# Kernel tuning notes

Hardware: AMD Instinct MI355X
Metric: run time of the kernel (lower is better)

Reference implementation:

```python
import jax, jax.numpy as jnp
import numpy as np

N_NODES = 10000
N_EDGES = 160000
N_FEAT = 512
HEADS = 8
HID = 128
OUT = 16


def setup_inputs() -> dict:
    key = jax.random.key(0)
    ks = jax.random.split(key, 16)
    inp = {
        'node_features': jax.random.normal(ks[0], (N_NODES, N_FEAT), jnp.float32),
        'edge_src': jax.random.randint(ks[1], (N_EDGES,), 0, N_NODES, jnp.int32),
        'edge_dst': jax.random.randint(ks[2], (N_EDGES,), 0, N_NODES, jnp.int32),
        # GAT layer params (scaled randn for numerical sanity)
        'W1': jax.random.normal(ks[3], (HEADS, HID, N_FEAT), jnp.float32) * 0.05,
        'a1': jax.random.normal(ks[4], (HEADS, 2 * HID), jnp.float32) * 0.05,
        'W2': jax.random.normal(ks[5], (HEADS, HID, HID), jnp.float32) * 0.05,
        'a2': jax.random.normal(ks[6], (HEADS, 2 * HID), jnp.float32) * 0.05,
        # MLP: LayerNorm(128) -> Linear(128,64) -> LeakyReLU -> Linear(64,16) -> LeakyReLU -> Linear(16,OUT) -> ReLU
        'ln_g': jnp.ones((HID,), jnp.float32),
        'ln_b': jnp.zeros((HID,), jnp.float32),
        'Wl1': jax.random.normal(ks[7], (64, HID), jnp.float32) * 0.05,
        'bl1': jnp.zeros((64,), jnp.float32),
        'Wl2': jax.random.normal(ks[8], (16, 64), jnp.float32) * 0.05,
        'bl2': jnp.zeros((16,), jnp.float32),
        'Wl3': jax.random.normal(ks[9], (OUT, 16), jnp.float32) * 0.05,
        'bl3': jnp.zeros((OUT,), jnp.float32),
    }
    return inp


def gat_layer(x, src, dst, W, a, n_nodes):
    # per-node, per-head projection: h[n,h,d]
    h = jnp.einsum('hdf,nf->nhd', W, x)
    # split attention vector: e_ij = a[:HID].h_i + a[HID:].h_j
    s_i = jnp.einsum('nhd,hd->nh', h, a[:, :HID])  # score contribution of target i
    s_j = jnp.einsum('nhd,hd->nh', h, a[:, HID:])  # score contribution of neighbor j
    e = jax.nn.leaky_relu(s_i[dst] + s_j[src])     # [E,H], negative_slope=0.01 (torch default)
    # segment softmax over edges grouped by dst
    m = jax.ops.segment_max(e, dst, num_segments=n_nodes)           # [N,H]
    m = jnp.where(jnp.isfinite(m), m, 0.0)
    ex = jnp.exp(e - m[dst])                                        # [E,H]
    denom = jax.ops.segment_sum(ex, dst, num_segments=n_nodes)      # [N,H]
    alpha = ex / jnp.where(denom > 0, denom, 1.0)[dst]              # [E,H]
    # scatter-accumulate weighted neighbor embeddings
    agg = jax.ops.segment_sum(alpha[:, :, None] * h[src], dst, num_segments=n_nodes)  # [N,H,HID]
    # average over heads, ELU (matches 1/attn_heads * attn_sum -> ELU)
    return jax.nn.elu(agg.mean(axis=1))  # [N,HID]


def reference(node_features, edge_src, edge_dst, W1, a1, W2, a2,
              ln_g, ln_b, Wl1, bl1, Wl2, bl2, Wl3, bl3):
    n = node_features.shape[0]
    emb1 = gat_layer(node_features, edge_src, edge_dst, W1, a1, n)
    emb2 = gat_layer(emb1, edge_src, edge_dst, W2, a2, n)
    g = emb2.mean(axis=0)  # [HID] graph embedding
    # MLP head (dropout = identity at inference)
    mu = g.mean()
    var = ((g - mu) ** 2).mean()
    gn = (g - mu) / jnp.sqrt(var + 1e-5) * ln_g + ln_b
    x = jax.nn.leaky_relu(Wl1 @ gn + bl1)
    x = jax.nn.leaky_relu(Wl2 @ x + bl2)
    return jax.nn.relu(Wl3 @ x + bl3)
```

## Files before the change

kernel.cpp:

```cpp
#include <hip/hip_runtime.h>
#include <math.h>

#define N_NODES 10000
#define N_EDGES 160000
#define N_FEAT  512
#define HEADS   8
#define HID     128

typedef __attribute__((ext_vector_type(8))) short bf16x8;
typedef __attribute__((ext_vector_type(4))) float f32x4;
typedef __attribute__((ext_vector_type(2))) float v2f;

__device__ inline unsigned short f2bf_rne(float f) {
  unsigned int u = __float_as_uint(f);
  unsigned int r = u + 0x7fffu + ((u >> 16) & 1u);
  return (unsigned short)(r >> 16);
}
__device__ inline float bf2f(unsigned int b) {
  return __uint_as_float(b << 16);
}

__device__ inline void split_body(const float* __restrict__ in,
                                  unsigned short* __restrict__ hi,
                                  int R, int K8, int idx) {
  int r = idx & 15;
  int t = idx >> 4;
  int kq = t % K8;
  int rb = t / K8;
  int row = rb * 16 + r;
  float v[8] = {0.f, 0.f, 0.f, 0.f, 0.f, 0.f, 0.f, 0.f};
  if (row < R) {
    const float* p = in + (size_t)row * (K8 * 8) + kq * 8;
    float4 a = *(const float4*)p;
    float4 b = *(const float4*)(p + 4);
    v[0] = a.x; v[1] = a.y; v[2] = a.z; v[3] = a.w;
    v[4] = b.x; v[5] = b.y; v[6] = b.z; v[7] = b.w;
  }
  union { unsigned short u[8]; int4 v4; } H;
  #pragma unroll
  for (int e = 0; e < 8; ++e) H.u[e] = f2bf_rne(v[e]);
  *(int4*)&hi[(size_t)idx * 8] = H.v4;
}

__global__ __launch_bounds__(256)
void split_frag2(const float* __restrict__ in1, unsigned short* __restrict__ hi1,
                 int R1, int K81, int total1, int nb1,
                 const float* __restrict__ in2, unsigned short* __restrict__ hi2,
                 int R2, int K82, int total2, int nb2,
                 const float* __restrict__ W2p, unsigned short* __restrict__ hi3,
                 int total3, int nb3,
                 const int* __restrict__ esrc, const int* __restrict__ edst,
                 int* __restrict__ deg, int* __restrict__ slots,
                 int2* __restrict__ ovf, int* __restrict__ cnt, int E,
                 const float* __restrict__ av1, const float* __restrict__ av2,
                 float* __restrict__ wt1, float* __restrict__ wt2) {
  int b = (int)blockIdx.x;
  int tid = threadIdx.x;
  if (b < nb1) {
    int idx = b * 256 + tid;
    if (idx < total1) split_body(in1, hi1, R1, K81, idx);
  } else if (b < nb1 + nb2) {
    int idx = (b - nb1) * 256 + tid;
    if (idx < total2) split_body(in2, hi2, R2, K82, idx);
  } else if (b < nb1 + nb2 + nb3) {
    int idx = (b - nb1 - nb2) * 256 + tid;
    if (idx < total3) split_body(W2p, hi3, HEADS * HID, 16, idx);
  } else {
    int nbE = (E + 255) / 256;
    int eb = b - nb1 - nb2 - nb3;
    if (eb < nbE) {
      int e = eb * 256 + tid;
      if (e < E) {
        int d = edst[e], s = esrc[e];
        int p = atomicAdd(&deg[d], 1);
        if (p < 32) {
          slots[d * 32 + p] = s;
        } else {
          int q = atomicAdd(&cnt[1], 1);
          if (q < E) ovf[q] = make_int2(d, s);
        }
      }
    } else {
      int wb = eb - nbE;
      if (wb < 32) {
        int o = wb * 256 + tid;
        int f = o & 511, ii = (o >> 9) & 1, h = o >> 10;
        const float* Wp = in2 + (size_t)h * HID * N_FEAT + f;
        const float* ap = av1 + h * 2 * HID + ii * HID;
        float c0 = 0.f, c1 = 0.f;
        for (int d = 0; d < HID; d += 2) {
          c0 = fmaf(Wp[(size_t)d * N_FEAT], ap[d], c0);
          c1 = fmaf(Wp[(size_t)(d + 1) * N_FEAT], ap[d + 1], c1);
        }
        wt1[o] = c0 + c1;
      } else {
        int o = (wb - 32) * 256 + tid;
        int f = o & 127, ii = (o >> 7) & 1, h = o >> 8;
        const float* Wp = W2p + (size_t)h * HID * HID + f;
        const float* ap = av2 + h * 2 * HID + ii * HID;
        float c0 = 0.f, c1 = 0.f;
        for (int d = 0; d < HID; d += 2) {
          c0 = fmaf(Wp[(size_t)d * HID], ap[d], c0);
          c1 = fmaf(Wp[(size_t)(d + 1) * HID], ap[d + 1], c1);
        }
        wt2[o] = c0 + c1;
      }
    }
  }
}

__global__ __launch_bounds__(256, 2)
void gemm_score(const unsigned short* __restrict__ Afh,
                const unsigned short* __restrict__ Bfh,
                unsigned short* __restrict__ hb,
                int M, int K, int nbGemm,
                const float* __restrict__ x, const float* __restrict__ wt1,
                float* __restrict__ si, float* __restrict__ sj, int N) {
  int tid = threadIdx.x;
  if ((int)blockIdx.x >= nbGemm) {
    __shared__ float wl[8192];
    #pragma unroll
    for (int k = 0; k < 32; ++k) wl[tid + k * 256] = wt1[tid + k * 256];
    __syncthreads();
    int wv = tid >> 6, lane = tid & 63;
    int rr = lane >> 4, sl = lane & 15;
    int n = ((int)blockIdx.x - nbGemm) * 16 + wv * 4 + rr;
    if (n >= N) return;
    const float* xp = x + (size_t)n * N_FEAT + sl * 4;
    float acc[16];
    #pragma unroll
    for (int t = 0; t < 16; ++t) acc[t] = 0.f;
    #pragma unroll
    for (int k = 0; k < 8; ++k) {
      float4 xv = *(const float4*)(xp + k * 64);
      #pragma unroll
      for (int t = 0; t < 16; ++t) {
        float4 w4 = *(const float4*)&wl[t * 512 + k * 64 + sl * 4];
        acc[t] = fmaf(xv.x, w4.x, fmaf(xv.y, w4.y, fmaf(xv.z, w4.z, fmaf(xv.w, w4.w, acc[t]))));
      }
    }
    #pragma unroll
    for (int o = 1; o <= 8; o <<= 1)
      #pragma unroll
      for (int t = 0; t < 16; ++t) acc[t] += __shfl_xor(acc[t], o);
    float outv = acc[0];
    #pragma unroll
    for (int t = 1; t < 16; ++t) outv = (sl == t) ? acc[t] : outv;
    int h = sl >> 1;
    if (sl & 1) sj[(size_t)h * N + n] = outv;
    else        si[(size_t)h * N + n] = outv;
    return;
  }

  int wave = tid >> 6, lane = tid & 63;
  int r = lane & 15, q = lane >> 4;
  int wr = wave >> 1, wc = wave & 1;

  int blk = blockIdx.x;
  int mtile = blk % 80;
  int head = blk / 80;
  int m0 = mtile * 128;
  int K8 = K >> 3;

  const bf16x8* pA = (const bf16x8*)Afh;
  const bf16x8* pB = (const bf16x8*)Bfh;
  size_t rstep = (size_t)K8 * 16;
  size_t aidx = (size_t)((m0 >> 4) + wr * 4) * rstep + (size_t)q * 16 + r;
  size_t bidx = (size_t)(head * 8 + wc * 4) * rstep + (size_t)q * 16 + r;

  f32x4 acc[4][4] = {};

  for (int k0 = 0; k0 < K; k0 += 128, aidx += 256, bidx += 256) {
    bf16x8 a[16], b[16];
    #pragma unroll
    for (int c = 0; c < 4; ++c)
      #pragma unroll
      for (int i = 0; i < 4; ++i) {
        a[c * 4 + i] = pA[aidx + i * rstep + c * 64];
        b[c * 4 + i] = pB[bidx + i * rstep + c * 64];
      }
    #pragma unroll
    for (int c = 0; c < 4; ++c)
      #pragma unroll
      for (int i = 0; i < 4; ++i)
        #pragma unroll
        for (int j = 0; j < 4; ++j)
          acc[i][j] = __builtin_amdgcn_mfma_f32_16x16x32_bf16(a[c * 4 + i], b[c * 4 + j], acc[i][j], 0, 0, 0);
  }

  #pragma unroll
  for (int i = 0; i < 4; ++i)
    #pragma unroll
    for (int reg = 0; reg < 4; ++reg) {
      int row = m0 + wr * 64 + i * 16 + q * 4 + reg;
      if (row < M) {
        #pragma unroll
        for (int j = 0; j < 4; ++j)
          hb[((size_t)head * M + row) * HID + wc * 64 + j * 16 + r] =
              f2bf_rne(acc[i][j][reg]);
      }
    }
}

__global__ __launch_bounds__(512)
void gat_aggregate9(const unsigned short* __restrict__ hb,
                    const float* __restrict__ si, const float* __restrict__ sj,
                    const int* __restrict__ deg, const int* __restrict__ slots,
                    const int2* __restrict__ ovf, const int* __restrict__ cnt,
                    unsigned short* __restrict__ aggb, int N) {
  __shared__ int2 prs[8][4][32];
  int head = blockIdx.x & 7;
  int wv = threadIdx.x >> 6;
  int lane = threadIdx.x & 63;
  int grp = lane >> 4;
  int sl = lane & 15;
  int n = (blockIdx.x >> 3) * 32 + wv * 4 + grp;
  const unsigned short* hbase = hb + (size_t)head * N * HID;
  const float* sjh = sj + (size_t)head * N;
  bool nv = n < N;
  int dg = 0;
  float s_i = 0.f;
  if (nv) {
    dg = deg[n];
    s_i = si[(size_t)head * N + n];
  }
  int sbase = n * 32;

  int src0 = 0, src1 = 0;
  float sc0 = -INFINITY, sc1 = -INFINITY;
  if (sl < dg) {
    src0 = slots[sbase + sl];
    float t = s_i + sjh[src0];
    sc0 = t > 0.f ? t : 0.01f * t;
  }
  if (16 + sl < dg) {
    src1 = slots[sbase + 16 + sl];
    float t = s_i + sjh[src1];
    sc1 = t > 0.f ? t : 0.01f * t;
  }
  float m = fmaxf(sc0, sc1);
  int oc = 0;
  if (dg > 32) {
    oc = cnt[1];
    if (oc > N_EDGES) oc = N_EDGES;
    for (int e2 = sl; e2 < oc; e2 += 16) {
      int2 pe = ovf[e2];
      if (pe.x == n) {
        float t = s_i + sjh[pe.y];
        t = t > 0.f ? t : 0.01f * t;
        m = fmaxf(m, t);
      }
    }
  }
  #pragma unroll
  for (int o = 1; o <= 8; o <<= 1) m = fmaxf(m, __shfl_xor(m, o));

  float w0 = (sl < dg) ? __expf(sc0 - m) : 0.f;
  float w1 = (16 + sl < dg) ? __expf(sc1 - m) : 0.f;
  float den = w0 + w1;
  if (dg > 32) {
    for (int e2 = sl; e2 < oc; e2 += 16) {
      int2 pe = ovf[e2];
      if (pe.x == n) {
        float t = s_i + sjh[pe.y];
        t = t > 0.f ? t : 0.01f * t;
        den += __expf(t - m);
      }
    }
  }
  #pragma unroll
  for (int o = 1; o <= 8; o <<= 1) den += __shfl_xor(den, o);

  prs[wv][grp][sl] = make_int2(src0, __float_as_int(w0));
  prs[wv][grp][16 + sl] = make_int2(src1, __float_as_int(w1));
  __asm__ volatile("s_waitcnt lgkmcnt(0)" ::: "memory");

  v2f a01 = {0.f, 0.f}, a23 = {0.f, 0.f}, a45 = {0.f, 0.f}, a67 = {0.f, 0.f};
  int dmin = dg < 32 ? dg : 32;
  for (int e0 = 0; e0 < dmin; e0 += 8) {
    int2 p[8];
    #pragma unroll
    for (int u = 0; u < 8; ++u) p[u] = prs[wv][grp][e0 + u];
    int4 pv[8];
    #pragma unroll
    for (int u = 0; u < 8; ++u)
      pv[u] = *(const int4*)&hbase[(size_t)p[u].x * HID + sl * 8];
    #pragma unroll
    for (int u = 0; u < 8; ++u) {
      float w = __int_as_float(p[u].y);
      v2f w2 = {w, w};
      int4 q = pv[u];
      v2f t0 = {bf2f((unsigned)q.x & 0xffffu), __uint_as_float((unsigned)q.x & 0xffff0000u)};
      v2f t1 = {bf2f((unsigned)q.y & 0xffffu), __uint_as_float((unsigned)q.y & 0xffff0000u)};
      v2f t2 = {bf2f((unsigned)q.z & 0xffffu), __uint_as_float((unsigned)q.z & 0xffff0000u)};
      v2f t3 = {bf2f((unsigned)q.w & 0xffffu), __uint_as_float((unsigned)q.w & 0xffff0000u)};
      a01 += w2 * t0;
      a23 += w2 * t1;
      a45 += w2 * t2;
      a67 += w2 * t3;
    }
  }
  if (dg > 32) {
    for (int e2 = 0; e2 < oc; ++e2) {
      int2 pe = ovf[e2];
      if (pe.x != n) continue;
      float t = s_i + sjh[pe.y];
      t = t > 0.f ? t : 0.01f * t;
      float w = __expf(t - m);
      v2f w2 = {w, w};
      int4 q = *(const int4*)&hbase[(size_t)pe.y * HID + sl * 8];
      v2f t0 = {bf2f((unsigned)q.x & 0xffffu), __uint_as_float((unsigned)q.x & 0xffff0000u)};
      v2f t1 = {bf2f((unsigned)q.y & 0xffffu), __uint_as_float((unsigned)q.y & 0xffff0000u)};
      v2f t2 = {bf2f((unsigned)q.z & 0xffffu), __uint_as_float((unsigned)q.z & 0xffff0000u)};
      v2f t3 = {bf2f((unsigned)q.w & 0xffffu), __uint_as_float((unsigned)q.w & 0xffff0000u)};
      a01 += w2 * t0; a23 += w2 * t1; a45 += w2 * t2; a67 += w2 * t3;
    }
  }

  if (nv) {
    float inv = den > 0.f ? 1.0f / den : 0.f;
    union { unsigned short u[8]; int4 v4; } P;
    P.u[0] = f2bf_rne(a01.x * inv); P.u[1] = f2bf_rne(a01.y * inv);
    P.u[2] = f2bf_rne(a23.x * inv); P.u[3] = f2bf_rne(a23.y * inv);
    P.u[4] = f2bf_rne(a45.x * inv); P.u[5] = f2bf_rne(a45.y * inv);
    P.u[6] = f2bf_rne(a67.x * inv); P.u[7] = f2bf_rne(a67.y * inv);
    *(int4*)&aggb[((size_t)head * N + n) * HID + sl * 8] = P.v4;
  }
}

__global__ __launch_bounds__(256)
void headmean_frag2(const unsigned short* __restrict__ aggb,
                    unsigned short* __restrict__ hiA, int N,
                    const float* __restrict__ wt2,
                    float* __restrict__ si, float* __restrict__ sj) {
  __shared__ float wl[2048];
  __shared__ float sred[16][16][17];
  int tid = threadIdx.x;
  #pragma unroll
  for (int k = 0; k < 8; ++k) wl[tid + k * 256] = wt2[tid + k * 256];
  __syncthreads();
  int idx = blockIdx.x * 256 + tid;
  int r = idx & 15;
  int kq = (idx >> 4) & 15;
  int rb = idx >> 8;
  int n = rb * 16 + r;
  float s[8] = {0.f, 0.f, 0.f, 0.f, 0.f, 0.f, 0.f, 0.f};
  if (n < N) {
    #pragma unroll
    for (int hh = 0; hh < HEADS; ++hh) {
      int4 pv = *(const int4*)&aggb[((size_t)hh * N + n) * HID + kq * 8];
      s[0] += bf2f((unsigned)pv.x & 0xffffu);
      s[1] += __uint_as_float((unsigned)pv.x & 0xffff0000u);
      s[2] += bf2f((unsigned)pv.y & 0xffffu);
      s[3] += __uint_as_float((unsigned)pv.y & 0xffff0000u);
      s[4] += bf2f((unsigned)pv.z & 0xffffu);
      s[5] += __uint_as_float((unsigned)pv.z & 0xffff0000u);
      s[6] += bf2f((unsigned)pv.w & 0xffffu);
      s[7] += __uint_as_float((unsigned)pv.w & 0xffff0000u);
    }
  }
  float p[16];
  #pragma unroll
  for (int t = 0; t < 16; ++t) p[t] = 0.f;
  union { unsigned short u[8]; int4 v4; } H;
  #pragma unroll
  for (int e = 0; e < 8; ++e) {
    float v = s[e] * (1.0f / HEADS);
    v = v > 0.f ? v : (__expf(v) - 1.0f);
    #pragma unroll
    for (int t = 0; t < 16; ++t) p[t] = fmaf(v, wl[t * 128 + kq * 8 + e], p[t]);
    H.u[e] = f2bf_rne(v);
  }
  *(int4*)&hiA[(size_t)idx * 8] = H.v4;
  #pragma unroll
  for (int t = 0; t < 16; ++t) sred[kq][r][t] = p[t];
  __syncthreads();
  {
    int rr = tid >> 4, t = tid & 15;
    float sum = 0.f;
    #pragma unroll
    for (int k = 0; k < 16; ++k) sum += sred[k][rr][t];
    int nn = rb * 16 + rr;
    if (nn < N) {
      int h = t >> 1;
      if (t & 1) sj[(size_t)h * N + nn] = sum;
      else       si[(size_t)h * N + nn] = sum;
    }
  }
}

__global__ __launch_bounds__(256)
void pool_mlp(const unsigned short* __restrict__ aggb, float* __restrict__ g,
              int N, int* __restrict__ cnt, int nbPool,
              const float* __restrict__ ln_g, const float* __restrict__ ln_b,
              const float* __restrict__ Wl1, const float* __restrict__ bl1,
              const float* __restrict__ Wl2, const float* __restrict__ bl2,
              const float* __restrict__ Wl3, const float* __restrict__ bl3,
              float* __restrict__ out, float invN) {
  __shared__ float sm[16][128];
  int t = threadIdx.x;
  int nl = t >> 4, dg = t & 15;
  int n = blockIdx.x * 16 + nl;
  float v[8] = {0.f, 0.f, 0.f, 0.f, 0.f, 0.f, 0.f, 0.f};
  if (n < N) {
    #pragma unroll
    for (int hh = 0; hh < HEADS; ++hh) {
      int4 pv = *(const int4*)&aggb[((size_t)hh * N + n) * HID + dg * 8];
      v[0] += bf2f((unsigned)pv.x & 0xffffu);
      v[1] += __uint_as_float((unsigned)pv.x & 0xffff0000u);
      v[2] += bf2f((unsigned)pv.y & 0xffffu);
      v[3] += __uint_as_float((unsigned)pv.y & 0xffff0000u);
      v[4] += bf2f((unsigned)pv.z & 0xffffu);
      v[5] += __uint_as_float((unsigned)pv.z & 0xffff0000u);
      v[6] += bf2f((unsigned)pv.w & 0xffffu);
      v[7] += __uint_as_float((unsigned)pv.w & 0xffff0000u);
    }
    #pragma unroll
    for (int e = 0; e < 8; ++e) {
      float x = v[e] * (1.0f / HEADS);
      v[e] = x > 0.f ? x : (__expf(x) - 1.0f);
    }
  }
  #pragma unroll
  for (int e = 0; e < 8; ++e) sm[nl][dg * 8 + e] = v[e];
  __syncthreads();
  if (t < 128) {
    float s = 0.f;
    #pragma unroll
    for (int nn = 0; nn < 16; ++nn) s += sm[nn][t];
    atomicAdd(&g[t], s);
  }
  __threadfence();
  __shared__ int lastFlag;
  if (t == 0) lastFlag = (atomicAdd(&cnt[0], 1) == nbPool - 1);
  __syncthreads();
  if (!lastFlag) return;

  __shared__ float red[128];
  __shared__ float gn[128];
  __shared__ float x1[64];
  __shared__ float x2[16];
  float gg = 0.f;
  if (t < 128) {
    gg = atomicAdd(&g[t], 0.f) * invN;
    red[t] = gg;
  }
  __syncthreads();
  for (int o = 64; o > 0; o >>= 1) {
    if (t < o) red[t] += red[t + o];
    __syncthreads();
  }
  float mu = red[0] * (1.0f / HID);
  __syncthreads();
  if (t < 128) {
    float dv = gg - mu;
    red[t] = dv * dv;
  }
  __syncthreads();
  for (int o = 64; o > 0; o >>= 1) {
    if (t < o) red[t] += red[t + o];
    __syncthreads();
  }
  float var = red[0] * (1.0f / HID);
  if (t < 128) gn[t] = (gg - mu) / sqrtf(var + 1e-5f) * ln_g[t] + ln_b[t];
  __syncthreads();
  if (t < 64) {
    float s = bl1[t];
    for (int k = 0; k < 128; ++k) s += Wl1[t * 128 + k] * gn[k];
    x1[t] = s > 0.f ? s : 0.01f * s;
  }
  __syncthreads();
  if (t < 16) {
    float s = bl2[t];
    for (int k = 0; k < 64; ++k) s += Wl2[t * 64 + k] * x1[k];
    x2[t] = s > 0.f ? s : 0.01f * s;
  }
  __syncthreads();
  if (t < 16) {
    float s = bl3[t];
    for (int k = 0; k < 16; ++k) s += Wl3[t * 16 + k] * x2[k];
    out[t] = s > 0.f ? s : 0.f;
  }
}

extern "C" void kernel_launch(void* const* d_in, const int* in_sizes, int n_in,
                              void* d_out, int out_size, void* d_ws, size_t ws_size,
                              hipStream_t stream) {
  const float* x    = (const float*)d_in[0];
  const int*   esrc = (const int*)d_in[1];
  const int*   edst = (const int*)d_in[2];
  const float* W1   = (const float*)d_in[3];
  const float* a1   = (const float*)d_in[4];
  const float* W2   = (const float*)d_in[5];
  const float* a2   = (const float*)d_in[6];
  const float* ln_g = (const float*)d_in[7];
  const float* ln_b = (const float*)d_in[8];
  const float* Wl1  = (const float*)d_in[9];
  const float* bl1  = (const float*)d_in[10];
  const float* Wl2  = (const float*)d_in[11];
  const float* bl2  = (const float*)d_in[12];
  const float* Wl3  = (const float*)d_in[13];
  const float* bl3  = (const float*)d_in[14];
  float* out = (float*)d_out;

  const int RBPAD = 640;

  unsigned short* aggb = (unsigned short*)d_ws;
  float* si   = (float*)(aggb + (size_t)N_NODES * HEADS * HID);
  float* sj   = si + N_NODES * HEADS;
  float* g    = sj + N_NODES * HEADS;
  int*   deg  = (int*)(g + 128);
  int*   cnt  = deg + N_NODES;
  int*   slots= cnt + 4;
  int2*  ovf  = (int2*)(slots + (size_t)N_NODES * 32);
  float* wt1  = (float*)(ovf + N_EDGES);
  float* wt2  = wt1 + 8192;
  unsigned short* Afh  = (unsigned short*)(wt2 + 2048);
  unsigned short* Bfh  = Afh + (size_t)RBPAD * 64 * 128;
  unsigned short* Bfh2 = Bfh + (size_t)1024 * 512;
  unsigned short* hb   = Bfh2 + (size_t)1024 * 128;

  hipMemsetAsync(g, 0, 128 * sizeof(float) + (N_NODES + 4) * sizeof(int), stream);

  int gemmGrid = 80 * HEADS;
  int scoreGrid = (N_NODES + 15) / 16;
  int aggGrid = ((N_NODES + 31) / 32) * 8;

  {
    int totalA = RBPAD * 64 * 16;
    int nbA = (totalA + 255) / 256;
    int totalB = 64 * 64 * 16;
    int nbB = (totalB + 255) / 256;
    int totalB2 = 64 * 16 * 16;
    int nbB2 = (totalB2 + 255) / 256;
    int nbE = (N_EDGES + 255) / 256;
    int nbW = 40;
    split_frag2<<<nbA + nbB + nbB2 + nbE + nbW, 256, 0, stream>>>(
        x, Afh, N_NODES, 64, totalA, nbA,
        W1, Bfh, HEADS * HID, 64, totalB, nbB,
        W2, Bfh2, totalB2, nbB2,
        esrc, edst, deg, slots, ovf, cnt, N_EDGES,
        a1, a2, wt1, wt2);
  }

  gemm_score<<<gemmGrid + scoreGrid, 256, 0, stream>>>(
      Afh, Bfh, hb, N_NODES, N_FEAT, gemmGrid, x, wt1, si, sj, N_NODES);
  gat_aggregate9<<<aggGrid, 512, 0, stream>>>(hb, si, sj, deg, slots, ovf, cnt,
                                              aggb, N_NODES);
  headmean_frag2<<<(N_NODES + 15) / 16, 256, 0, stream>>>(aggb, Afh, N_NODES,
                                                          wt2, si, sj);

  gemm_score<<<gemmGrid, 256, 0, stream>>>(
      Afh, Bfh2, hb, N_NODES, HID, gemmGrid, nullptr, nullptr, nullptr, nullptr, 0);
  gat_aggregate9<<<aggGrid, 512, 0, stream>>>(hb, si, sj, deg, slots, ovf, cnt,
                                              aggb, N_NODES);

  {
    int nbPool = (N_NODES + 15) / 16;
    pool_mlp<<<nbPool, 256, 0, stream>>>(aggb, g, N_NODES, cnt, nbPool,
                                         ln_g, ln_b, Wl1, bl1, Wl2, bl2,
                                         Wl3, bl3, out, 1.0f / N_NODES);
  }
}
```

Baseline: 271.5 us.

## Fuse aggregation with head-mean and pooling via cooperative persistent kernels

Replaces the separate aggregate, head-mean and pool/MLP launches with two cooperative persistent kernels that loop over work items and use grid-wide syncs between phases. The goal is to cut kernel launch gaps and the last-block atomic counter pattern. In exchange, the grid is capped at occupancy times 256 blocks, which may reduce latency hiding for the gather-heavy aggregation. Grid.sync and cooperative launch also add their own overhead. The head-mean output is now written in a fragment index layout that must match what the following GEMM expects.

Measured after the change: 399.8 us. +47.3%, slower.

```diff
diff --git a/kernel.cpp b/kernel.cpp
--- a/kernel.cpp
+++ b/kernel.cpp
@@ -1,5 +1,8 @@
 #include <hip/hip_runtime.h>
+#include <hip/hip_cooperative_groups.h>
 #include <math.h>
+
+namespace cg = cooperative_groups;
 
 #define N_NODES 10000
 #define N_EDGES 160000
@@ -202,284 +205,317 @@
     }
 }
 
-__global__ __launch_bounds__(512)
-void gat_aggregate9(const unsigned short* __restrict__ hb,
-                    const float* __restrict__ si, const float* __restrict__ sj,
-                    const int* __restrict__ deg, const int* __restrict__ slots,
-                    const int2* __restrict__ ovf, const int* __restrict__ cnt,
-                    unsigned short* __restrict__ aggb, int N) {
-  __shared__ int2 prs[8][4][32];
-  int head = blockIdx.x & 7;
-  int wv = threadIdx.x >> 6;
-  int lane = threadIdx.x & 63;
+__device__ inline void agg_phase(const unsigned short* __restrict__ hb,
+                                 const float* __restrict__ si,
+                                 const float* __restrict__ sj,
+                                 const int* __restrict__ deg,
+                                 const int* __restrict__ slots,
+                                 const int2* __restrict__ ovf,
+                                 const int* __restrict__ cnt,
+                                 unsigned short* __restrict__ aggb,
+                                 char* smem, int tid, int bid, int nblk) {
+  int2 (*prs)[4][32] = (int2 (*)[4][32])smem;
+  int wv = tid >> 6;
+  int lane = tid & 63;
   int grp = lane >> 4;
   int sl = lane & 15;
-  int n = (blockIdx.x >> 3) * 32 + wv * 4 + grp;
-  const unsigned short* hbase = hb + (size_t)head * N * HID;
-  const float* sjh = sj + (size_t)head * N;
-  bool nv = n < N;
-  int dg = 0;
-  float s_i = 0.f;
-  if (nv) {
-    dg = deg[n];
-    s_i = si[(size_t)head * N + n];
-  }
-  int sbase = n * 32;
-
-  int src0 = 0, src1 = 0;
-  float sc0 = -INFINITY, sc1 = -INFINITY;
-  if (sl < dg) {
-    src0 = slots[sbase + sl];
-    float t = s_i + sjh[src0];
-    sc0 = t > 0.f ? t : 0.01f * t;
-  }
-  if (16 + sl < dg) {
-    src1 = slots[sbase + 16 + sl];
-    float t = s_i + sjh[src1];
-    sc1 = t > 0.f ? t : 0.01f * t;
-  }
-  float m = fmaxf(sc0, sc1);
-  int oc = 0;
-  if (dg > 32) {
-    oc = cnt[1];
-    if (oc > N_EDGES) oc = N_EDGES;
-    for (int e2 = sl; e2 < oc; e2 += 16) {
-      int2 pe = ovf[e2];
-      if (pe.x == n) {
+  for (int vb = bid; vb < 313 * 8; vb += nblk) {
+    int head = vb & 7;
+    int n = (vb >> 3) * 32 + wv * 4 + grp;
+    const unsigned short* hbase = hb + (size_t)head * N_NODES * HID;
+    const float* sjh = sj + (size_t)head * N_NODES;
+    bool nv = n < N_NODES;
+    int dg = 0;
+    float s_i = 0.f;
+    if (nv) {
+      dg = deg[n];
+      s_i = si[(size_t)head * N_NODES + n];
+    }
+    int sbase = n * 32;
+
+    int src0 = 0, src1 = 0;
+    float sc0 = -INFINITY, sc1 = -INFINITY;
+    if (sl < dg) {
+      src0 = slots[sbase + sl];
+      float t = s_i + sjh[src0];
+      sc0 = t > 0.f ? t : 0.01f * t;
+    }
+    if (16 + sl < dg) {
+      src1 = slots[sbase + 16 + sl];
+      float t = s_i + sjh[src1];
+      sc1 = t > 0.f ? t : 0.01f * t;
+    }
+    float m = fmaxf(sc0, sc1);
+    int oc = 0;
+    if (dg > 32) {
+      oc = cnt[1];
+      if (oc > N_EDGES) oc = N_EDGES;
+      for (int e2 = sl; e2 < oc; e2 += 16) {
+        int2 pe = ovf[e2];
+        if (pe.x == n) {
+          float t = s_i + sjh[pe.y];
+          t = t > 0.f ? t : 0.01f * t;
+          m = fmaxf(m, t);
+        }
+      }
+    }
+    #pragma unroll
+    for (int o = 1; o <= 8; o <<= 1) m = fmaxf(m, __shfl_xor(m, o));
+
+    float w0 = (sl < dg) ? __expf(sc0 - m) : 0.f;
+    float w1 = (16 + sl < dg) ? __expf(sc1 - m) : 0.f;
+    float den = w0 + w1;
+    if (dg > 32) {
+      for (int e2 = sl; e2 < oc; e2 += 16) {
+        int2 pe = ovf[e2];
+        if (pe.x == n) {
+          float t = s_i + sjh[pe.y];
+          t = t > 0.f ? t : 0.01f * t;
+          den += __expf(t - m);
+        }
+      }
+    }
+    #pragma unroll
+    for (int o = 1; o <= 8; o <<= 1) den += __shfl_xor(den, o);
+
+    prs[wv][grp][sl] = make_int2(src0, __float_as_int(w0));
+    prs[wv][grp][16 + sl] = make_int2(src1, __float_as_int(w1));
+    __asm__ volatile("s_waitcnt lgkmcnt(0)" ::: "memory");
+
+    v2f a01 = {0.f, 0.f}, a23 = {0.f, 0.f}, a45 = {0.f, 0.f}, a67 = {0.f, 0.f};
+    int dmin = dg < 32 ? dg : 32;
+    for (int e0 = 0; e0 < dmin; e0 += 8) {
+      int2 p[8];
+      #pragma unroll
+      for (int u = 0; u < 8; ++u) p[u] = prs[wv][grp][e0 + u];
+      int4 pv[8];
+      #pragma unroll
+      for (int u = 0; u < 8; ++u)
+        pv[u] = *(const int4*)&hbase[(size_t)p[u].x * HID + sl * 8];
+      #pragma unroll
+      for (int u = 0; u < 8; ++u) {
+        float w = __int_as_float(p[u].y);
+        v2f w2 = {w, w};
+        int4 q = pv[u];
+        v2f t0 = {bf2f((unsigned)q.x & 0xffffu), __uint_as_float((unsigned)q.x & 0xffff0000u)};
+        v2f t1 = {bf2f((unsigned)q.y & 0xffffu), __uint_as_float((unsigned)q.y & 0xffff0000u)};
+        v2f t2 = {bf2f((unsigned)q.z & 0xffffu), __uint_as_float((unsigned)q.z & 0xffff0000u)};
+        v2f t3 = {bf2f((unsigned)q.w & 0xffffu), __uint_as_float((unsigned)q.w & 0xffff0000u)};
+        a01 += w2 * t0;
+        a23 += w2 * t1;
+        a45 += w2 * t2;
+        a67 += w2 * t3;
+      }
+    }
+    if (dg > 32) {
+      for (int e2 = 0; e2 < oc; ++e2) {
+        int2 pe = ovf[e2];
+        if (pe.x != n) continue;
         float t = s_i + sjh[pe.y];
         t = t > 0.f ? t : 0.01f * t;
-        m = fmaxf(m, t);
-      }
-    }
-  }
-  #pragma unroll
-  for (int o = 1; o <= 8; o <<= 1) m = fmaxf(m, __shfl_xor(m, o));
-
-  float w0 = (sl < dg) ? __expf(sc0 - m) : 0.f;
-  float w1 = (16 + sl < dg) ? __expf(sc1 - m) : 0.f;
-  float den = w0 + w1;
-  if (dg > 32) {
-    for (int e2 = sl; e2 < oc; e2 += 16) {
-      int2 pe = ovf[e2];
-      if (pe.x == n) {
-        float t = s_i + sjh[pe.y];
-        t = t > 0.f ? t : 0.01f * t;
-        den += __expf(t - m);
-      }
-    }
-  }
-  #pragma unroll
-  for (int o = 1; o <= 8; o <<= 1) den += __shfl_xor(den, o);
-
-  prs[wv][grp][sl] = make_int2(src0, __float_as_int(w0));
-  prs[wv][grp][16 + sl] = make_int2(src1, __float_as_int(w1));
-  __asm__ volatile("s_waitcnt lgkmcnt(0)" ::: "memory");
-
-  v2f a01 = {0.f, 0.f}, a23 = {0.f, 0.f}, a45 = {0.f, 0.f}, a67 = {0.f, 0.f};
-  int dmin = dg < 32 ? dg : 32;
-  for (int e0 = 0; e0 < dmin; e0 += 8) {
-    int2 p[8];
-    #pragma unroll
-    for (int u = 0; u < 8; ++u) p[u] = prs[wv][grp][e0 + u];
-    int4 pv[8];
-    #pragma unroll
-    for (int u = 0; u < 8; ++u)
-      pv[u] = *(const int4*)&hbase[(size_t)p[u].x * HID + sl * 8];
-    #pragma unroll
-    for (int u = 0; u < 8; ++u) {
-      float w = __int_as_float(p[u].y);
-      v2f w2 = {w, w};
-      int4 q = pv[u];
-      v2f t0 = {bf2f((unsigned)q.x & 0xffffu), __uint_as_float((unsigned)q.x & 0xffff0000u)};
-      v2f t1 = {bf2f((unsigned)q.y & 0xffffu), __uint_as_float((unsigned)q.y & 0xffff0000u)};
-      v2f t2 = {bf2f((unsigned)q.z & 0xffffu), __uint_as_float((unsigned)q.z & 0xffff0000u)};
-      v2f t3 = {bf2f((unsigned)q.w & 0xffffu), __uint_as_float((unsigned)q.w & 0xffff0000u)};
-      a01 += w2 * t0;
-      a23 += w2 * t1;
-      a45 += w2 * t2;
-      a67 += w2 * t3;
-    }
-  }
-  if (dg > 32) {
-    for (int e2 = 0; e2 < oc; ++e2) {
-      int2 pe = ovf[e2];
-      if (pe.x != n) continue;
-      float t = s_i + sjh[pe.y];
-      t = t > 0.f ? t : 0.01f * t;
-      float w = __expf(t - m);
-      v2f w2 = {w, w};
-      int4 q = *(const int4*)&hbase[(size_t)pe.y * HID + sl * 8];
-      v2f t0 = {bf2f((unsigned)q.x & 0xffffu), __uint_as_float((unsigned)q.x & 0xffff0000u)};
-      v2f t1 = {bf2f((unsigned)q.y & 0xffffu), __uint_as_float((unsigned)q.y & 0xffff0000u)};
-      v2f t2 = {bf2f((unsigned)q.z & 0xffffu), __uint_as_float((unsigned)q.z & 0xffff0000u)};
-      v2f t3 = {bf2f((unsigned)q.w & 0xffffu), __uint_as_float((unsigned)q.w & 0xffff0000u)};
-      a01 += w2 * t0; a23 += w2 * t1; a45 += w2 * t2; a67 += w2 * t3;
-    }
-  }
-
-  if (nv) {
-    float inv = den > 0.f ? 1.0f / den : 0.f;
-    union { unsigned short u[8]; int4 v4; } P;
-    P.u[0] = f2bf_rne(a01.x * inv); P.u[1] = f2bf_rne(a01.y * inv);
-    P.u[2] = f2bf_rne(a23.x * inv); P.u[3] = f2bf_rne(a23.y * inv);
-    P.u[4] = f2bf_rne(a45.x * inv); P.u[5] = f2bf_rne(a45.y * inv);
-    P.u[6] = f2bf_rne(a67.x * inv); P.u[7] = f2bf_rne(a67.y * inv);
-    *(int4*)&aggb[((size_t)head * N + n) * HID + sl * 8] = P.v4;
-  }
-}
-
-__global__ __launch_bounds__(256)
-void headmean_frag2(const unsigned short* __restrict__ aggb,
-                    unsigned short* __restrict__ hiA, int N,
-                    const float* __restrict__ wt2,
-                    float* __restrict__ si, float* __restrict__ sj) {
-  __shared__ float wl[2048];
-  __shared__ float sred[16][16][17];
-  int tid = threadIdx.x;
-  #pragma unroll
-  for (int k = 0; k < 8; ++k) wl[tid + k * 256] = wt2[tid + k * 256];
-  __syncthreads();
-  int idx = blockIdx.x * 256 + tid;
-  int r = idx & 15;
-  int kq = (idx >> 4) & 15;
-  int rb = idx >> 8;
-  int n = rb * 16 + r;
-  float s[8] = {0.f, 0.f, 0.f, 0.f, 0.f, 0.f, 0.f, 0.f};
-  if (n < N) {
-    #pragma unroll
-    for (int hh = 0; hh < HEADS; ++hh) {
-      int4 pv = *(const int4*)&aggb[((size_t)hh * N + n) * HID + kq * 8];
-      s[0] += bf2f((unsigned)pv.x & 0xffffu);
-      s[1] += __uint_as_float((unsigned)pv.x & 0xffff0000u);
-      s[2] += bf2f((unsigned)pv.y & 0xffffu);
-      s[3] += __uint_as_float((unsigned)pv.y & 0xffff0000u);
-      s[4] += bf2f((unsigned)pv.z & 0xffffu);
-      s[5] += __uint_as_float((unsigned)pv.z & 0xffff0000u);
-      s[6] += bf2f((unsigned)pv.w & 0xffffu);
-      s[7] += __uint_as_float((unsigned)pv.w & 0xffff0000u);
-    }
-  }
-  float p[16];
-  #pragma unroll
-  for (int t = 0; t < 16; ++t) p[t] = 0.f;
-  union { unsigned short u[8]; int4 v4; } H;
-  #pragma unroll
-  for (int e = 0; e < 8; ++e) {
-    float v = s[e] * (1.0f / HEADS);
-    v = v > 0.f ? v : (__expf(v) - 1.0f);
-    #pragma unroll
-    for (int t = 0; t < 16; ++t) p[t] = fmaf(v, wl[t * 128 + kq * 8 + e], p[t]);
-    H.u[e] = f2bf_rne(v);
-  }
-  *(int4*)&hiA[(size_t)idx * 8] = H.v4;
-  #pragma unroll
-  for (int t = 0; t < 16; ++t) sred[kq][r][t] = p[t];
-  __syncthreads();
+        float w = __expf(t - m);
+        v2f w2 = {w, w};
+        int4 q = *(const int4*)&hbase[(size_t)pe.y * HID + sl * 8];
+        v2f t0 = {bf2f((unsigned)q.x & 0xffffu), __uint_as_float((unsigned)q.x & 0xffff0000u)};
+        v2f t1 = {bf2f((unsigned)q.y & 0xffffu), __uint_as_float((unsigned)q.y & 0xffff0000u)};
+        v2f t2 = {bf2f((unsigned)q.z & 0xffffu), __uint_as_float((unsigned)q.z & 0xffff0000u)};
+        v2f t3 = {bf2f((unsigned)q.w & 0xffffu), __uint_as_float((unsigned)q.w & 0xffff0000u)};
+        a01 += w2 * t0; a23 += w2 * t1; a45 += w2 * t2; a67 += w2 * t3;
+      }
+    }
+
+    if (nv) {
+      float inv = den > 0.f ? 1.0f / den : 0.f;
+      union { unsigned short u[8]; int4 v4; } P;
+      P.u[0] = f2bf_rne(a01.x * inv); P.u[1] = f2bf_rne(a01.y * inv);
+      P.u[2] = f2bf_rne(a23.x * inv); P.u[3] = f2bf_rne(a23.y * inv);
+      P.u[4] = f2bf_rne(a45.x * inv); P.u[5] = f2bf_rne(a45.y * inv);
+      P.u[6] = f2bf_rne(a67.x * inv); P.u[7] = f2bf_rne(a67.y * inv);
+      *(int4*)&aggb[((size_t)head * N_NODES + n) * HID + sl * 8] = P.v4;
+    }
+  }
+}
+
+__global__ __launch_bounds__(512, 1)
+void coop_agg_hm(const unsigned short* __restrict__ hb,
+                 float* __restrict__ si, float* __restrict__ sj,
+                 const int* __restrict__ deg, const int* __restrict__ slots,
+                 const int2* __restrict__ ovf, const int* __restrict__ cnt,
+                 unsigned short* __restrict__ aggb,
+                 unsigned short* __restrict__ Afh,
+                 const float* __restrict__ wt2) {
+  __shared__ __align__(16) char smem[43008];
+  cg::grid_group grid = cg::this_grid();
+  const int tid = threadIdx.x;
+  const int bid = blockIdx.x;
+  const int nblk = gridDim.x;
+
+  agg_phase(hb, si, sj, deg, slots, ovf, cnt, aggb, smem, tid, bid, nblk);
+  grid.sync();
+
   {
-    int rr = tid >> 4, t = tid & 15;
-    float sum = 0.f;
-    #pragma unroll
-    for (int k = 0; k < 16; ++k) sum += sred[k][rr][t];
-    int nn = rb * 16 + rr;
-    if (nn < N) {
-      int h = t >> 1;
-      if (t & 1) sj[(size_t)h * N + nn] = sum;
-      else       si[(size_t)h * N + nn] = sum;
-    }
-  }
-}
-
-__global__ __launch_bounds__(256)
-void pool_mlp(const unsigned short* __restrict__ aggb, float* __restrict__ g,
-              int N, int* __restrict__ cnt, int nbPool,
-              const float* __restrict__ ln_g, const float* __restrict__ ln_b,
-              const float* __restrict__ Wl1, const float* __restrict__ bl1,
-              const float* __restrict__ Wl2, const float* __restrict__ bl2,
-              const float* __restrict__ Wl3, const float* __restrict__ bl3,
-              float* __restrict__ out, float invN) {
-  __shared__ float sm[16][128];
-  int t = threadIdx.x;
-  int nl = t >> 4, dg = t & 15;
-  int n = blockIdx.x * 16 + nl;
-  float v[8] = {0.f, 0.f, 0.f, 0.f, 0.f, 0.f, 0.f, 0.f};
-  if (n < N) {
-    #pragma unroll
-    for (int hh = 0; hh < HEADS; ++hh) {
-      int4 pv = *(const int4*)&aggb[((size_t)hh * N + n) * HID + dg * 8];
-      v[0] += bf2f((unsigned)pv.x & 0xffffu);
-      v[1] += __uint_as_float((unsigned)pv.x & 0xffff0000u);
-      v[2] += bf2f((unsigned)pv.y & 0xffffu);
-      v[3] += __uint_as_float((unsigned)pv.y & 0xffff0000u);
-      v[4] += bf2f((unsigned)pv.z & 0xffffu);
-      v[5] += __uint_as_float((unsigned)pv.z & 0xffff0000u);
-      v[6] += bf2f((unsigned)pv.w & 0xffffu);
-      v[7] += __uint_as_float((unsigned)pv.w & 0xffff0000u);
-    }
-    #pragma unroll
-    for (int e = 0; e < 8; ++e) {
-      float x = v[e] * (1.0f / HEADS);
-      v[e] = x > 0.f ? x : (__expf(x) - 1.0f);
-    }
-  }
-  #pragma unroll
-  for (int e = 0; e < 8; ++e) sm[nl][dg * 8 + e] = v[e];
-  __syncthreads();
-  if (t < 128) {
-    float s = 0.f;
-    #pragma unroll
-    for (int nn = 0; nn < 16; ++nn) s += sm[nn][t];
-    atomicAdd(&g[t], s);
-  }
-  __threadfence();
-  __shared__ int lastFlag;
-  if (t == 0) lastFlag = (atomicAdd(&cnt[0], 1) == nbPool - 1);
-  __syncthreads();
-  if (!lastFlag) return;
-
-  __shared__ float red[128];
-  __shared__ float gn[128];
-  __shared__ float x1[64];
-  __shared__ float x2[16];
-  float gg = 0.f;
-  if (t < 128) {
-    gg = atomicAdd(&g[t], 0.f) * invN;
-    red[t] = gg;
-  }
-  __syncthreads();
-  for (int o = 64; o > 0; o >>= 1) {
-    if (t < o) red[t] += red[t + o];
-    __syncthreads();
-  }
-  float mu = red[0] * (1.0f / HID);
-  __syncthreads();
-  if (t < 128) {
-    float dv = gg - mu;
-    red[t] = dv * dv;
-  }
-  __syncthreads();
-  for (int o = 64; o > 0; o >>= 1) {
-    if (t < o) red[t] += red[t + o];
-    __syncthreads();
-  }
-  float var = red[0] * (1.0f / HID);
-  if (t < 128) gn[t] = (gg - mu) / sqrtf(var + 1e-5f) * ln_g[t] + ln_b[t];
-  __syncthreads();
-  if (t < 64) {
-    float s = bl1[t];
-    for (int k = 0; k < 128; ++k) s += Wl1[t * 128 + k] * gn[k];
-    x1[t] = s > 0.f ? s : 0.01f * s;
-  }
-  __syncthreads();
-  if (t < 16) {
-    float s = bl2[t];
-    for (int k = 0; k < 64; ++k) s += Wl2[t * 64 + k] * x1[k];
-    x2[t] = s > 0.f ? s : 0.01f * s;
-  }
-  __syncthreads();
-  if (t < 16) {
-    float s = bl3[t];
-    for (int k = 0; k < 16; ++k) s += Wl3[t * 16 + k] * x2[k];
-    out[t] = s > 0.f ? s : 0.f;
+    float* wl2 = (float*)smem;
+    float (*sred)[32][17] = (float (*)[32][17])(smem + 8192);
+    for (int k = tid; k < 2048; k += 512) wl2[k] = wt2[k];
+    __syncthreads();
+    int kq = tid >> 5, r32 = tid & 31;
+    for (int vb = bid; vb < 313; vb += nblk) {
+      int n = vb * 32 + r32;
+      float s[8] = {0.f, 0.f, 0.f, 0.f, 0.f, 0.f, 0.f, 0.f};
+      if (n < N_NODES) {
+        #pragma unroll
+        for (int hh = 0; hh < HEADS; ++hh) {
+          int4 pv = *(const int4*)&aggb[((size_t)hh * N_NODES + n) * HID + kq * 8];
+          s[0] += bf2f((unsigned)pv.x & 0xffffu);
+          s[1] += __uint_as_float((unsigned)pv.x & 0xffff0000u);
+          s[2] += bf2f((unsigned)pv.y & 0xffffu);
+          s[3] += __uint_as_float((unsigned)pv.y & 0xffff0000u);
+          s[4] += bf2f((unsigned)pv.z & 0xffffu);
+          s[5] += __uint_as_float((unsigned)pv.z & 0xffff0000u);
+          s[6] += bf2f((unsigned)pv.w & 0xffffu);
+          s[7] += __uint_as_float((unsigned)pv.w & 0xffff0000u);
+        }
+      }
+      float p[16];
+      #pragma unroll
+      for (int t = 0; t < 16; ++t) p[t] = 0.f;
+      union { unsigned short u[8]; int4 v4; } H;
+      #pragma unroll
+      for (int e = 0; e < 8; ++e) {
+        float v = s[e] * (1.0f / HEADS);
+        v = v > 0.f ? v : (__expf(v) - 1.0f);
+        #pragma unroll
+        for (int t = 0; t < 16; ++t) p[t] = fmaf(v, wl2[t * 128 + kq * 8 + e], p[t]);
+        H.u[e] = f2bf_rne(v);
+      }
+      if (n < N_NODES) {
+        size_t idx = ((size_t)(n >> 4) * 16 + kq) * 16 + (n & 15);
+        *(int4*)&Afh[idx * 8] = H.v4;
+      }
+      #pragma unroll
+      for (int t = 0; t < 16; ++t) sred[kq][r32][t] = p[t];
+      __syncthreads();
+      {
+        int rr = tid >> 4, t = tid & 15;
+        float sum = 0.f;
+        #pragma unroll
+        for (int k = 0; k < 16; ++k) sum += sred[k][rr][t];
+        int nn = vb * 32 + rr;
+        if (nn < N_NODES) {
+          int h = t >> 1;
+          if (t & 1) sj[(size_t)h * N_NODES + nn] = sum;
+          else       si[(size_t)h * N_NODES + nn] = sum;
+        }
+      }
+      __syncthreads();
+    }
+  }
+}
+
+__global__ __launch_bounds__(512, 1)
+void coop_agg_pool_mlp(const unsigned short* __restrict__ hb,
+                       const float* __restrict__ si, const float* __restrict__ sj,
+                       const int* __restrict__ deg, const int* __restrict__ slots,
+                       const int2* __restrict__ ovf, const int* __restrict__ cnt,
+                       unsigned short* __restrict__ aggb, float* __restrict__ g,
+                       const float* __restrict__ ln_g, const float* __restrict__ ln_b,
+                       const float* __restrict__ Wl1, const float* __restrict__ bl1,
+                       const float* __restrict__ Wl2, const float* __restrict__ bl2,
+                       const float* __restrict__ Wl3, const float* __restrict__ bl3,
+                       float* __restrict__ out) {
+  __shared__ __align__(16) char smem[16384];
+  cg::grid_group grid = cg::this_grid();
+  const int tid = threadIdx.x;
+  const int bid = blockIdx.x;
+  const int nblk = gridDim.x;
+
+  agg_phase(hb, si, sj, deg, slots, ovf, cnt, aggb, smem, tid, bid, nblk);
+  grid.sync();
+
+  {
+    float (*sm)[128] = (float (*)[128])smem;
+    int nl = tid >> 4, dgx = tid & 15;
+    for (int vb = bid; vb < 313; vb += nblk) {
+      int n = vb * 32 + nl;
+      float v[8] = {0.f, 0.f, 0.f, 0.f, 0.f, 0.f, 0.f, 0.f};
+      if (n < N_NODES) {
+        #pragma unroll
+        for (int hh = 0; hh < HEADS; ++hh) {
+          int4 pv = *(const int4*)&aggb[((size_t)hh * N_NODES + n) * HID + dgx * 8];
+          v[0] += bf2f((unsigned)pv.x & 0xffffu);
+          v[1] += __uint_as_float((unsigned)pv.x & 0xffff0000u);
+          v[2] += bf2f((unsigned)pv.y & 0xffffu);
+          v[3] += __uint_as_float((unsigned)pv.y & 0xffff0000u);
+          v[4] += bf2f((unsigned)pv.z & 0xffffu);
+          v[5] += __uint_as_float((unsigned)pv.z & 0xffff0000u);
+          v[6] += bf2f((unsigned)pv.w & 0xffffu);
+          v[7] += __uint_as_float((unsigned)pv.w & 0xffff0000u);
+        }
+        #pragma unroll
+        for (int e = 0; e < 8; ++e) {
+          float xv = v[e] * (1.0f / HEADS);
+          v[e] = xv > 0.f ? xv : (__expf(xv) - 1.0f);
+        }
+      }
+      #pragma unroll
+      for (int e = 0; e < 8; ++e) sm[nl][dgx * 8 + e] = v[e];
+      __syncthreads();
+      if (tid < 128) {
+        float s = 0.f;
+        #pragma unroll
+        for (int nn = 0; nn < 32; ++nn) s += sm[nn][tid];
+        atomicAdd(&g[tid], s);
+      }
+      __syncthreads();
+    }
+  }
+  grid.sync();
+
+  if (bid == 0) {
+    float* red = (float*)smem;
+    float* gnb = red + 128;
+    float* x1 = gnb + 128;
+    float* x2 = x1 + 64;
+    int t = tid;
+    float gg = 0.f;
+    if (t < 128) {
+      gg = g[t] * (1.0f / N_NODES);
+      red[t] = gg;
+    }
+    __syncthreads();
+    for (int o = 64; o > 0; o >>= 1) {
+      if (t < o) red[t] += red[t + o];
+      __syncthreads();
+    }
+    float mu = red[0] * (1.0f / HID);
+    __syncthreads();
+    if (t < 128) red[t] = (gg - mu) * (gg - mu);
+    __syncthreads();
+    for (int o = 64; o > 0; o >>= 1) {
+      if (t < o) red[t] += red[t + o];
+      __syncthreads();
+    }
+    float var = red[0] * (1.0f / HID);
+    __syncthreads();
+    if (t < 128) gnb[t] = (gg - mu) / sqrtf(var + 1e-5f) * ln_g[t] + ln_b[t];
+    __syncthreads();
+    if (t < 64) {
+      float s = bl1[t];
+      for (int k = 0; k < 128; ++k) s += Wl1[t * 128 + k] * gnb[k];
+      x1[t] = s > 0.f ? s : 0.01f * s;
+    }
+    __syncthreads();
+    if (t < 16) {
+      float s = bl2[t];
+      for (int k = 0; k < 64; ++k) s += Wl2[t * 64 + k] * x1[k];
+      x2[t] = s > 0.f ? s : 0.01f * s;
+    }
+    __syncthreads();
+    if (t < 16) {
+      float s = bl3[t];
+      for (int k = 0; k < 16; ++k) s += Wl3[t * 16 + k] * x2[k];
+      out[t] = s > 0.f ? s : 0.f;
+    }
   }
 }
 
@@ -524,7 +560,6 @@
 
   int gemmGrid = 80 * HEADS;
   int scoreGrid = (N_NODES + 15) / 16;
-  int aggGrid = ((N_NODES + 31) / 32) * 8;
 
   {
     int totalA = RBPAD * 64 * 16;
@@ -545,20 +580,37 @@
 
   gemm_score<<<gemmGrid + scoreGrid, 256, 0, stream>>>(
       Afh, Bfh, hb, N_NODES, N_FEAT, gemmGrid, x, wt1, si, sj, N_NODES);
-  gat_aggregate9<<<aggGrid, 512, 0, stream>>>(hb, si, sj, deg, slots, ovf, cnt,
-                                              aggb, N_NODES);
-  headmean_frag2<<<(N_NODES + 15) / 16, 256, 0, stream>>>(aggb, Afh, N_NODES,
-                                                          wt2, si, sj);
+
+  {
+    int maxB = 0;
+    if (hipOccupancyMaxActiveBlocksPerMultiprocessor(&maxB, coop_agg_hm, 512, 0)
+            != hipSuccess || maxB < 1)
+      maxB = 1;
+    int gridA = maxB * 256;
+    void* argsA[] = {
+      (void*)&hb, (void*)&si, (void*)&sj, (void*)&deg, (void*)&slots,
+      (void*)&ovf, (void*)&cnt, (void*)&aggb, (void*)&Afh, (void*)&wt2
+    };
+    hipLaunchCooperativeKernel((const void*)coop_agg_hm, dim3(gridA), dim3(512),
+                               argsA, 0, stream);
+  }
 
   gemm_score<<<gemmGrid, 256, 0, stream>>>(
       Afh, Bfh2, hb, N_NODES, HID, gemmGrid, nullptr, nullptr, nullptr, nullptr, 0);
-  gat_aggregate9<<<aggGrid, 512, 0, stream>>>(hb, si, sj, deg, slots, ovf, cnt,
-                                              aggb, N_NODES);
 
   {
-    int nbPool = (N_NODES + 15) / 16;
-    pool_mlp<<<nbPool, 256, 0, stream>>>(aggb, g, N_NODES, cnt, nbPool,
-                                         ln_g, ln_b, Wl1, bl1, Wl2, bl2,
-                                         Wl3, bl3, out, 1.0f / N_NODES);
-  }
-}
+    int maxB = 0;
+    if (hipOccupancyMaxActiveBlocksPerMultiprocessor(&maxB, coop_agg_pool_mlp, 512, 0)
+            != hipSuccess || maxB < 1)
+      maxB = 1;
+    int gridB = maxB * 256;
+    void* argsB[] = {
+      (void*)&hb, (void*)&si, (void*)&sj, (void*)&deg, (void*)&slots,
+      (void*)&ovf, (void*)&cnt, (void*)&aggb, (void*)&g,
+      (void*)&ln_g, (void*)&ln_b, (void*)&Wl1, (void*)&bl1,
+      (void*)&Wl2, (void*)&bl2, (void*)&Wl3, (void*)&bl3, (void*)&out
+    };
+    hipLaunchCooperativeKernel((const void*)coop_agg_pool_mlp, dim3(gridB), dim3(512),
+                               argsB, 0, stream);
+  }
+}
```
